# Kernel optimization log

Hardware: AMD Instinct MI355X
Metric: run time of the kernel (lower is better)

Reference implementation:

```python
import jax, jax.numpy as jnp
import numpy as np

D_MODEL = 256
N_HEADS = 8
N_LEVELS = 4
NUM_POINTS_LIST = [4, 4, 4, 4]
SUM_POINTS = sum(NUM_POINTS_LIST)
TOTAL_POINTS = N_HEADS * SUM_POINTS
HEAD_DIM = D_MODEL // N_HEADS
OFFSET_SCALE = 0.5
SPATIAL_SHAPES = np.array([[80, 80], [40, 40], [20, 20], [10, 10]], dtype=np.int64)


def setup_inputs() -> dict:
    key = jax.random.key(0)
    ks = jax.random.split(key, 7)
    B, NQ = 16, 300
    seq = int((SPATIAL_SHAPES[:, 0] * SPATIAL_SHAPES[:, 1]).sum())  # 8500
    s = 1.0 / np.sqrt(D_MODEL)
    return {
        'hidden_states': jax.random.normal(ks[0], (B, NQ, D_MODEL), jnp.float32),
        'encoder_hidden_states': jax.random.normal(ks[1], (B, seq, D_MODEL), jnp.float32),
        'reference_points': jax.random.uniform(ks[2], (B, NQ, 1, 4), jnp.float32, 0.05, 0.95),
        'spatial_shapes': SPATIAL_SHAPES,
        'w_off': jax.random.uniform(ks[3], (TOTAL_POINTS * 2, D_MODEL), jnp.float32, -s, s),
        'b_off': jax.random.uniform(ks[4], (TOTAL_POINTS * 2,), jnp.float32, -s, s),
        'w_attn': jax.random.uniform(ks[5], (TOTAL_POINTS, D_MODEL), jnp.float32, -s, s),
        'b_attn': jax.random.uniform(ks[6], (TOTAL_POINTS,), jnp.float32, -s, s),
    }


def _grid_sample_zeros(img_flat, H, W, gx, gy):
    # img_flat: [N, H*W, C]; gx, gy: [N, Q, P] unnormalized pixel coords.
    # Bilinear, padding_mode='zeros', align_corners=False semantics of torch.grid_sample.
    x0 = jnp.floor(gx)
    y0 = jnp.floor(gy)
    wx = (gx - x0)[..., None]
    wy = (gy - y0)[..., None]
    x0i = x0.astype(jnp.int32)
    y0i = y0.astype(jnp.int32)

    def gather(xi, yi):
        valid = (xi >= 0) & (xi < W) & (yi >= 0) & (yi < H)
        idx = jnp.clip(yi, 0, H - 1) * W + jnp.clip(xi, 0, W - 1)
        N = img_flat.shape[0]
        v = jnp.take_along_axis(img_flat, idx.reshape(N, -1)[..., None], axis=1)
        v = v.reshape(idx.shape + (img_flat.shape[-1],))
        return v * valid[..., None]

    v00 = gather(x0i, y0i)
    v01 = gather(x0i + 1, y0i)
    v10 = gather(x0i, y0i + 1)
    v11 = gather(x0i + 1, y0i + 1)
    top = v00 * (1 - wx) + v01 * wx
    bot = v10 * (1 - wx) + v11 * wx
    return top * (1 - wy) + bot * wy  # [N, Q, P, C]


def reference(hidden_states, encoder_hidden_states, reference_points, spatial_shapes, w_off, b_off, w_attn, b_attn):
    B, NQ, _ = hidden_states.shape
    seq = encoder_hidden_states.shape[1]
    shapes = np.asarray(spatial_shapes)

    value = encoder_hidden_states.reshape(B, seq, N_HEADS, HEAD_DIM)

    off = (hidden_states @ w_off.T + b_off).reshape(B, NQ, N_HEADS, SUM_POINTS, 2)
    attn = jax.nn.softmax((hidden_states @ w_attn.T + b_attn).reshape(B, NQ, N_HEADS, SUM_POINTS), axis=-1)

    # reference_points: [B, NQ, 1, 4] (cx, cy, w, h) in [0,1]
    nps = jnp.asarray(np.repeat([1.0 / n for n in NUM_POINTS_LIST], NUM_POINTS_LIST), hidden_states.dtype)[:, None]
    offset = off * nps * reference_points[:, :, None, :, 2:] * OFFSET_SCALE
    sampling_locations = reference_points[:, :, None, :, :2] + offset  # [B,NQ,H,P,2]

    grids = 2.0 * sampling_locations - 1.0
    value_bh = value.transpose(0, 2, 1, 3).reshape(B * N_HEADS, seq, HEAD_DIM)
    grids_bh = grids.transpose(0, 2, 1, 3, 4).reshape(B * N_HEADS, NQ, SUM_POINTS, 2)

    outs = []
    start_s, start_p = 0, 0
    for lvl in range(N_LEVELS):
        Hl, Wl = int(shapes[lvl, 0]), int(shapes[lvl, 1])
        Pl = NUM_POINTS_LIST[lvl]
        img = value_bh[:, start_s:start_s + Hl * Wl]  # [BH, Hl*Wl, hd]
        g = grids_bh[:, :, start_p:start_p + Pl]
        gx = (g[..., 0] + 1.0) * Wl / 2.0 - 0.5
        gy = (g[..., 1] + 1.0) * Hl / 2.0 - 0.5
        outs.append(_grid_sample_zeros(img, Hl, Wl, gx, gy))
        start_s += Hl * Wl
        start_p += Pl

    sampled = jnp.concatenate(outs, axis=2)  # [BH, NQ, SUM_POINTS, hd]
    attn_bh = attn.transpose(0, 2, 1, 3).reshape(B * N_HEADS, NQ, SUM_POINTS, 1)
    out = (sampled * attn_bh).sum(axis=2)  # [BH, NQ, hd]
    out = out.reshape(B, N_HEADS, NQ, HEAD_DIM).transpose(0, 2, 1, 3).reshape(B, NQ, D_MODEL)
    return (out, attn)
```

## Files before the change

### kernel.cpp

```cpp
#include <hip/hip_runtime.h>
#include <hip/hip_bf16.h>

#define BQ_TOTAL 4800
#define D_MODEL 256
#define N_HEADS 8
#define SUM_POINTS 16
#define HEAD_DIM 32
#define SEQ 8500
#define OUT_ELEMS (BQ_TOTAL * D_MODEL)

#define BM 64
#define BN 64
#define BK 32
#define PAD 4

__global__ __launch_bounds__(256) void gemm_logits(
    const float* __restrict__ hs,
    const float* __restrict__ w_off, const float* __restrict__ b_off,
    const float* __restrict__ w_attn, const float* __restrict__ b_attn,
    float* __restrict__ off_out, float* __restrict__ attn_out)
{
    __shared__ float As[BK][BM + PAD];
    __shared__ float Bs[BK][BN + PAD];

    const int tid = threadIdx.x;
    const int row0 = blockIdx.x * BM;
    const int col0 = blockIdx.y * BN;

    const float* Bsrc; const float* bias; int bcol;
    if (col0 < 256) { Bsrc = w_off;  bias = b_off;  bcol = col0; }
    else            { Bsrc = w_attn; bias = b_attn; bcol = col0 - 256; }

    const int tx = tid & 15;
    const int ty = tid >> 4;
    const int lrow = tid >> 3;
    const int k4 = (tid & 7) * 4;

    float acc[4][4] = {};

    for (int k0 = 0; k0 < 256; k0 += BK) {
        #pragma unroll
        for (int rr = 0; rr < 2; rr++) {
            const int r = lrow + rr * 32;
            const float4 a = *(const float4*)(hs + (size_t)(row0 + r) * 256 + k0 + k4);
            As[k4 + 0][r] = a.x; As[k4 + 1][r] = a.y;
            As[k4 + 2][r] = a.z; As[k4 + 3][r] = a.w;
            const float4 b = *(const float4*)(Bsrc + (size_t)(bcol + r) * 256 + k0 + k4);
            Bs[k4 + 0][r] = b.x; Bs[k4 + 1][r] = b.y;
            Bs[k4 + 2][r] = b.z; Bs[k4 + 3][r] = b.w;
        }
        __syncthreads();
        #pragma unroll
        for (int kk = 0; kk < BK; kk++) {
            const float4 av = *(const float4*)&As[kk][ty * 4];
            const float4 bv = *(const float4*)&Bs[kk][tx * 4];
            const float af[4] = {av.x, av.y, av.z, av.w};
            const float bf[4] = {bv.x, bv.y, bv.z, bv.w};
            #pragma unroll
            for (int i = 0; i < 4; i++)
                #pragma unroll
                for (int j = 0; j < 4; j++)
                    acc[i][j] += af[i] * bf[j];
        }
        __syncthreads();
    }

    #pragma unroll
    for (int i = 0; i < 4; i++) {
        const int r = row0 + ty * 4 + i;
        const int c_local = tx * 4;
        float4 v;
        v.x = acc[i][0] + bias[bcol + c_local + 0];
        v.y = acc[i][1] + bias[bcol + c_local + 1];
        v.z = acc[i][2] + bias[bcol + c_local + 2];
        v.w = acc[i][3] + bias[bcol + c_local + 3];
        if (col0 < 256)
            *(float4*)(off_out + (size_t)r * 256 + col0 + c_local) = v;
        else
            *(float4*)(attn_out + (size_t)r * 128 + (col0 - 256) + c_local) = v;
    }
}

__global__ __launch_bounds__(256) void deform_sample(
    const float* __restrict__ enc,
    const float* __restrict__ refp,
    const float* __restrict__ offlog,
    float* __restrict__ attn,
    float* __restrict__ out)
{
    const int tid = threadIdx.x;
    const int w = tid >> 6;
    const int lane = tid & 63;
    const int item = blockIdx.x * 4 + w;
    const int bq = item >> 3;
    const int h = item & 7;
    const int p = lane >> 2;
    const int sub = lane & 3;

    float* attn_ptr = attn + (size_t)bq * 128 + h * 16;
    const float l = attn_ptr[p];
    float m = l;
    #pragma unroll
    for (int s = 4; s < 64; s <<= 1) m = fmaxf(m, __shfl_xor(m, s));
    const float e = __expf(l - m);
    float ssum = e;
    #pragma unroll
    for (int s = 4; s < 64; s <<= 1) ssum += __shfl_xor(ssum, s);
    const float prob = e / ssum;
    if (sub == 0) attn_ptr[p] = prob;

    const float2 off2 = *(const float2*)(offlog + (size_t)bq * 256 + h * 32 + 2 * p);
    const float* rp = refp + (size_t)bq * 4;
    const float cx = rp[0], cy = rp[1], rw = rp[2], rh = rp[3];

    const int lvl = p >> 2;
    const int Wl = 80 >> lvl;
    int base = 0;
    if (lvl == 1) base = 6400;
    else if (lvl == 2) base = 8000;
    else if (lvl == 3) base = 8400;

    const float Wf = (float)Wl;
    const float gx = (cx + off2.x * 0.125f * rw) * Wf - 0.5f;
    const float gy = (cy + off2.y * 0.125f * rh) * Wf - 0.5f;
    const float x0f = floorf(gx), y0f = floorf(gy);
    const float fx = gx - x0f, fy = gy - y0f;
    const int x0 = (int)x0f, y0 = (int)y0f;

    const int b = bq / 300;
    const float* pbase = enc + ((size_t)b * SEQ + base) * 256 + h * 32 + sub * 4;

    float4 acc0 = {0.f, 0.f, 0.f, 0.f};
    float4 acc1 = {0.f, 0.f, 0.f, 0.f};
    #pragma unroll
    for (int c = 0; c < 4; c++) {
        const int xc = x0 + (c & 1);
        const int yc = y0 + (c >> 1);
        const float wx = (c & 1) ? fx : (1.0f - fx);
        const float wy = (c >> 1) ? fy : (1.0f - fy);
        const bool valid = (xc >= 0) && (xc < Wl) && (yc >= 0) && (yc < Wl);
        const int xi = min(max(xc, 0), Wl - 1);
        const int yi = min(max(yc, 0), Wl - 1);
        const float wgt = valid ? wx * wy : 0.0f;
        const float* vp = pbase + (size_t)(yi * Wl + xi) * 256;
        const float4 va = *(const float4*)(vp);
        const float4 vb = *(const float4*)(vp + 16);
        acc0.x += wgt * va.x; acc0.y += wgt * va.y;
        acc0.z += wgt * va.z; acc0.w += wgt * va.w;
        acc1.x += wgt * vb.x; acc1.y += wgt * vb.y;
        acc1.z += wgt * vb.z; acc1.w += wgt * vb.w;
    }

    float vals[8];
    vals[0] = acc0.x * prob; vals[1] = acc0.y * prob;
    vals[2] = acc0.z * prob; vals[3] = acc0.w * prob;
    vals[4] = acc1.x * prob; vals[5] = acc1.y * prob;
    vals[6] = acc1.z * prob; vals[7] = acc1.w * prob;

    #pragma unroll
    for (int s = 4; s < 64; s <<= 1) {
        #pragma unroll
        for (int j = 0; j < 8; j++) vals[j] += __shfl_xor(vals[j], s);
    }

    if (lane < 8) {
        const int halfs = lane >> 2;
        const int sb = lane & 3;
        float4 v;
        if (halfs == 0) { v.x = vals[0]; v.y = vals[1]; v.z = vals[2]; v.w = vals[3]; }
        else            { v.x = vals[4]; v.y = vals[5]; v.z = vals[6]; v.w = vals[7]; }
        out[(size_t)bq * 256 + h * 32 + halfs * 16 + sb * 4 + 0] = v.x;
        out[(size_t)bq * 256 + h * 32 + halfs * 16 + sb * 4 + 1] = v.y;
        out[(size_t)bq * 256 + h * 32 + halfs * 16 + sb * 4 + 2] = v.z;
        out[(size_t)bq * 256 + h * 32 + halfs * 16 + sb * 4 + 3] = v.w;
    }
}

extern "C" void kernel_launch(void* const* d_in, const int* in_sizes, int n_in,
                              void* d_out, int out_size, void* d_ws, size_t ws_size,
                              hipStream_t stream) {
    const float* hs     = (const float*)d_in[0];
    const float* enc    = (const float*)d_in[1];
    const float* refp   = (const float*)d_in[2];
    const float* w_off  = (const float*)d_in[4];
    const float* b_off  = (const float*)d_in[5];
    const float* w_attn = (const float*)d_in[6];
    const float* b_attn = (const float*)d_in[7];

    float* out  = (float*)d_out;
    float* attn = out + OUT_ELEMS;
    float* offlog = (float*)d_ws;

    dim3 g1(BQ_TOTAL / BM, 384 / BN);
    gemm_logits<<<g1, 256, 0, stream>>>(hs, w_off, b_off, w_attn, b_attn, offlog, attn);

    deform_sample<<<(BQ_TOTAL * N_HEADS) / 4, 256, 0, stream>>>(enc, refp, offlog, attn, out);
}
```

Baseline: 231.4 us.

## Use fp16 MFMA for the offset/attention logit GEMM

Replaces the scalar FP32 tiled GEMM that computes offset and attention logits with one that converts both operands to fp16 in shared memory and runs 16x16x32 MFMA instructions. The whole K=256 slab is loaded at once with a padded stride, so there is a single barrier instead of one per K-step. This cuts ALU time in the GEMM stage. It lowers input precision to fp16, which perturbs the sampling offsets and the softmax inputs, and the output stores become scalar, strided writes.

After: 216.9 us. -6.3%, faster.

```diff
diff --git a/kernel.cpp b/kernel.cpp
--- a/kernel.cpp
+++ b/kernel.cpp
@@ -9,75 +9,80 @@
 #define SEQ 8500
 #define OUT_ELEMS (BQ_TOTAL * D_MODEL)
 
-#define BM 64
-#define BN 64
-#define BK 32
-#define PAD 4
-
-__global__ __launch_bounds__(256) void gemm_logits(
+typedef _Float16 half8 __attribute__((ext_vector_type(8)));
+typedef _Float16 half4 __attribute__((ext_vector_type(4)));
+typedef float floatx4 __attribute__((ext_vector_type(4)));
+
+#define LDK 264
+
+__global__ __launch_bounds__(256) void gemm_logits_mfma(
     const float* __restrict__ hs,
     const float* __restrict__ w_off, const float* __restrict__ b_off,
     const float* __restrict__ w_attn, const float* __restrict__ b_attn,
     float* __restrict__ off_out, float* __restrict__ attn_out)
 {
-    __shared__ float As[BK][BM + PAD];
-    __shared__ float Bs[BK][BN + PAD];
+    __shared__ _Float16 Asld[64 * LDK];
+    __shared__ _Float16 Bsld[64 * LDK];
 
     const int tid = threadIdx.x;
-    const int row0 = blockIdx.x * BM;
-    const int col0 = blockIdx.y * BN;
-
-    const float* Bsrc; const float* bias; int bcol;
-    if (col0 < 256) { Bsrc = w_off;  bias = b_off;  bcol = col0; }
-    else            { Bsrc = w_attn; bias = b_attn; bcol = col0 - 256; }
-
-    const int tx = tid & 15;
-    const int ty = tid >> 4;
-    const int lrow = tid >> 3;
-    const int k4 = (tid & 7) * 4;
-
-    float acc[4][4] = {};
-
-    for (int k0 = 0; k0 < 256; k0 += BK) {
+    const int row0 = blockIdx.x * 64;
+    const int col0 = blockIdx.y * 64;
+
+    const float* Bsrc; const float* bias;
+    if (col0 < 256) { Bsrc = w_off  + (size_t)col0 * 256;        bias = b_off  + col0; }
+    else            { Bsrc = w_attn + (size_t)(col0 - 256) * 256; bias = b_attn + (col0 - 256); }
+
+    #pragma unroll
+    for (int i = 0; i < 16; i++) {
+        const int idx = tid + i * 256;
+        const int r = idx >> 6;
+        const int kc = (idx & 63) << 2;
+
+        const float4 a = *(const float4*)(hs + (size_t)(row0 + r) * 256 + kc);
+        half4 ah; ah[0] = (_Float16)a.x; ah[1] = (_Float16)a.y;
+                  ah[2] = (_Float16)a.z; ah[3] = (_Float16)a.w;
+        *(half4*)&Asld[r * LDK + kc] = ah;
+
+        const float4 b = *(const float4*)(Bsrc + (size_t)r * 256 + kc);
+        half4 bh; bh[0] = (_Float16)b.x; bh[1] = (_Float16)b.y;
+                  bh[2] = (_Float16)b.z; bh[3] = (_Float16)b.w;
+        *(half4*)&Bsld[r * LDK + kc] = bh;
+    }
+    __syncthreads();
+
+    const int wv = tid >> 6;
+    const int lane = tid & 63;
+    const int m = lane & 15;
+    const int quad = lane >> 4;
+
+    half8 af[8];
+    #pragma unroll
+    for (int q8 = 0; q8 < 8; q8++)
+        af[q8] = *(const half8*)&Asld[(wv * 16 + m) * LDK + q8 * 32 + quad * 8];
+
+    floatx4 acc[4] = {{0.f,0.f,0.f,0.f},{0.f,0.f,0.f,0.f},{0.f,0.f,0.f,0.f},{0.f,0.f,0.f,0.f}};
+    #pragma unroll
+    for (int ct = 0; ct < 4; ct++) {
         #pragma unroll
-        for (int rr = 0; rr < 2; rr++) {
-            const int r = lrow + rr * 32;
-            const float4 a = *(const float4*)(hs + (size_t)(row0 + r) * 256 + k0 + k4);
-            As[k4 + 0][r] = a.x; As[k4 + 1][r] = a.y;
-            As[k4 + 2][r] = a.z; As[k4 + 3][r] = a.w;
-            const float4 b = *(const float4*)(Bsrc + (size_t)(bcol + r) * 256 + k0 + k4);
-            Bs[k4 + 0][r] = b.x; Bs[k4 + 1][r] = b.y;
-            Bs[k4 + 2][r] = b.z; Bs[k4 + 3][r] = b.w;
+        for (int q8 = 0; q8 < 8; q8++) {
+            const half8 bf = *(const half8*)&Bsld[(ct * 16 + m) * LDK + q8 * 32 + quad * 8];
+            acc[ct] = __builtin_amdgcn_mfma_f32_16x16x32_f16(af[q8], bf, acc[ct], 0, 0, 0);
         }
-        __syncthreads();
+    }
+
+    #pragma unroll
+    for (int ct = 0; ct < 4; ct++) {
+        const int col_l = ct * 16 + m;
+        const float bv = bias[col_l];
         #pragma unroll
-        for (int kk = 0; kk < BK; kk++) {
-            const float4 av = *(const float4*)&As[kk][ty * 4];
-            const float4 bv = *(const float4*)&Bs[kk][tx * 4];
-            const float af[4] = {av.x, av.y, av.z, av.w};
-            const float bf[4] = {bv.x, bv.y, bv.z, bv.w};
-            #pragma unroll
-            for (int i = 0; i < 4; i++)
-                #pragma unroll
-                for (int j = 0; j < 4; j++)
-                    acc[i][j] += af[i] * bf[j];
+        for (int rg = 0; rg < 4; rg++) {
+            const int row = row0 + wv * 16 + quad * 4 + rg;
+            const float v = acc[ct][rg] + bv;
+            if (col0 < 256)
+                off_out[(size_t)row * 256 + col0 + col_l] = v;
+            else
+                attn_out[(size_t)row * 128 + (col0 - 256) + col_l] = v;
         }
-        __syncthreads();
-    }
-
-    #pragma unroll
-    for (int i = 0; i < 4; i++) {
-        const int r = row0 + ty * 4 + i;
-        const int c_local = tx * 4;
-        float4 v;
-        v.x = acc[i][0] + bias[bcol + c_local + 0];
-        v.y = acc[i][1] + bias[bcol + c_local + 1];
-        v.z = acc[i][2] + bias[bcol + c_local + 2];
-        v.w = acc[i][3] + bias[bcol + c_local + 3];
-        if (col0 < 256)
-            *(float4*)(off_out + (size_t)r * 256 + col0 + c_local) = v;
-        else
-            *(float4*)(attn_out + (size_t)r * 128 + (col0 - 256) + c_local) = v;
     }
 }
 
@@ -191,8 +196,8 @@
     float* attn = out + OUT_ELEMS;
     float* offlog = (float*)d_ws;
 
-    dim3 g1(BQ_TOTAL / BM, 384 / BN);
-    gemm_logits<<<g1, 256, 0, stream>>>(hs, w_off, b_off, w_attn, b_attn, offlog, attn);
+    dim3 g1(BQ_TOTAL / 64, 384 / 64);
+    gemm_logits_mfma<<<g1, 256, 0, stream>>>(hs, w_off, b_off, w_attn, b_attn, offlog, attn);
 
     deform_sample<<<(BQ_TOTAL * N_HEADS) / 4, 256, 0, stream>>>(enc, refp, offlog, attn, out);
 }
```
